# Kernel optimization log

Measured on AMD Instinct MI355X. Metric: run time of the kernel, lower is better.

Reference implementation:

```python
import jax, jax.numpy as jnp
import numpy as np

N, E, G = 20000, 600000, 128
NF, HID, L, H = 16, 128, 4, 4
C = HID // H  # 32 per-head out dim
BN_EPS = 1e-5


def setup_inputs() -> dict:
    key = jax.random.key(0)
    ks = jax.random.split(key, 24)
    inp = {}
    inp['x'] = jax.random.normal(ks[0], (N, NF), dtype=jnp.float32)
    inp['edge_index'] = jax.random.randint(ks[1], (2, E), 0, N, dtype=jnp.int32)
    inp['batch'] = jnp.sort(jax.random.randint(ks[2], (N,), 0, G, dtype=jnp.int32))
    s = 0.05
    inp['emb_w'] = jax.random.normal(ks[3], (NF, HID), dtype=jnp.float32) * s
    inp['emb_b'] = jnp.zeros((HID,), dtype=jnp.float32)
    inp['gat_w'] = jax.random.normal(ks[4], (L, HID, HID), dtype=jnp.float32) * s
    inp['att_src'] = jax.random.normal(ks[5], (L, H, C), dtype=jnp.float32) * s
    inp['att_dst'] = jax.random.normal(ks[6], (L, H, C), dtype=jnp.float32) * s
    inp['gat_b'] = jnp.zeros((L, HID), dtype=jnp.float32)
    inp['bn_gamma'] = jnp.ones((L, HID), dtype=jnp.float32)
    inp['bn_beta'] = jnp.zeros((L, HID), dtype=jnp.float32)
    inp['bn_mean'] = jax.random.normal(ks[7], (L, HID), dtype=jnp.float32) * 0.01
    inp['bn_var'] = jnp.ones((L, HID), dtype=jnp.float32)
    inp['fc1_w'] = jax.random.normal(ks[8], (HID, 64), dtype=jnp.float32) * s
    inp['fc1_b'] = jnp.zeros((64,), dtype=jnp.float32)
    inp['fc2_w'] = jax.random.normal(ks[9], (64, 32), dtype=jnp.float32) * s
    inp['fc2_b'] = jnp.zeros((32,), dtype=jnp.float32)
    inp['bg_w'] = jax.random.normal(ks[10], (32, 1), dtype=jnp.float32) * s
    inp['bg_b'] = jnp.zeros((1,), dtype=jnp.float32)
    return inp


def _gat_layer(x, W, a_src, a_dst, bias, src, dst):
    # PyG GATConv (concat=True, negative_slope=0.2, self-loops already appended)
    h = (x @ W).reshape(N, H, C)                      # [N,H,C]
    s_src = jnp.sum(h * a_src, axis=-1)               # [N,H]
    s_dst = jnp.sum(h * a_dst, axis=-1)               # [N,H]
    e = jax.nn.leaky_relu(s_src[src] + s_dst[dst], 0.2)  # [E+N,H]
    m = jax.ops.segment_max(e, dst, num_segments=N)   # per-dest softmax max
    ex = jnp.exp(e - m[dst])
    denom = jax.ops.segment_sum(ex, dst, num_segments=N)
    alpha = ex / (denom[dst] + 1e-16)                 # [E+N,H]
    msg = h[src] * alpha[:, :, None]                  # [E+N,H,C]
    out = jax.ops.segment_sum(msg, dst, num_segments=N)
    return out.reshape(N, HID) + bias


def reference(x, edge_index, batch, emb_w, emb_b, gat_w, att_src, att_dst, gat_b,
              bn_gamma, bn_beta, bn_mean, bn_var, fc1_w, fc1_b, fc2_w, fc2_b, bg_w, bg_b):
    # add self loops (PyG GATConv default)
    loops = jnp.arange(N, dtype=edge_index.dtype)
    src = jnp.concatenate([edge_index[0], loops])
    dst = jnp.concatenate([edge_index[1], loops])

    h = jax.nn.relu(x @ emb_w + emb_b)
    for l in range(L):
        hn = _gat_layer(h, gat_w[l], att_src[l], att_dst[l], gat_b[l], src, dst)
        hn = (hn - bn_mean[l]) * (bn_gamma[l] / jnp.sqrt(bn_var[l] + BN_EPS)) + bn_beta[l]
        h = h + jax.nn.relu(hn)

    # global mean pool over graphs
    sums = jax.ops.segment_sum(h, batch, num_segments=G)
    cnts = jax.ops.segment_sum(jnp.ones((N,), dtype=h.dtype), batch, num_segments=G)
    g = sums / jnp.maximum(cnts, 1.0)[:, None]        # [G,HID]

    g = jax.nn.relu(g @ fc1_w + fc1_b)
    g = jax.nn.relu(g @ fc2_w + fc2_b)
    out = g @ bg_w + bg_b                              # band_gap head
    return out.squeeze(-1)                             # [G]
```

## Files before the change

### kernel.cpp

```cpp
#include <hip/hip_runtime.h>
#include <math.h>

#define HID 128
#define NF  16
#define NH  4
#define HC  32
#define NLAYERS 4

__global__ void k_count_init(int* __restrict__ counts, int N) {
    int i = blockIdx.x * blockDim.x + threadIdx.x;
    if (i < N) counts[i] = 1;
}

__global__ void k_count_edges(const int* __restrict__ dst, int E, int* __restrict__ counts) {
    int i = blockIdx.x * blockDim.x + threadIdx.x;
    if (i < E) atomicAdd(&counts[dst[i]], 1);
}

__global__ __launch_bounds__(1024) void k_scan(const int* __restrict__ counts,
                                               int* __restrict__ row_ptr, int N) {
    __shared__ int sums[1024];
    const int t = threadIdx.x;
    const int per = (N + 1023) >> 10;
    const int beg = min(t * per, N);
    const int end = min(beg + per, N);
    int s = 0;
    for (int i = beg; i < end; ++i) s += counts[i];
    sums[t] = s;
    __syncthreads();
    for (int off = 1; off < 1024; off <<= 1) {
        int v = (t >= off) ? sums[t - off] : 0;
        __syncthreads();
        sums[t] += v;
        __syncthreads();
    }
    int run = sums[t] - s;
    for (int i = beg; i < end; ++i) { row_ptr[i] = run; run += counts[i]; }
    if (t == 1023) row_ptr[N] = sums[1023];
}

__global__ void k_selfloop(const int* __restrict__ row_ptr, int* __restrict__ col,
                           int* __restrict__ fill, int N) {
    int i = blockIdx.x * blockDim.x + threadIdx.x;
    if (i < N) { col[row_ptr[i]] = i; fill[i] = 1; }
}

__global__ void k_scatter(const int* __restrict__ src, const int* __restrict__ dst, int E,
                          const int* __restrict__ row_ptr, int* __restrict__ fill,
                          int* __restrict__ col) {
    int i = blockIdx.x * blockDim.x + threadIdx.x;
    if (i < E) {
        int d = dst[i];
        int pos = atomicAdd(&fill[d], 1);
        col[row_ptr[d] + pos] = src[i];
    }
}

__global__ void k_bnprep(const float* __restrict__ gat_b, const float* __restrict__ gamma,
                         const float* __restrict__ beta, const float* __restrict__ mean,
                         const float* __restrict__ var,
                         float* __restrict__ scale, float* __restrict__ shift) {
    int i = blockIdx.x * blockDim.x + threadIdx.x;
    if (i < NLAYERS * HID) {
        float sc = gamma[i] / sqrtf(var[i] + 1e-5f);
        scale[i] = sc;
        shift[i] = beta[i] + (gat_b[i] - mean[i]) * sc;
    }
}

__global__ __launch_bounds__(256) void k_embed(const float* __restrict__ x,
                                               const float* __restrict__ w,
                                               const float* __restrict__ b,
                                               float* __restrict__ h, int N) {
    __shared__ float ws_[NF * HID];
    __shared__ float bs[HID];
    const int t = threadIdx.x;
    for (int i = t; i < NF * HID; i += 256) ws_[i] = w[i];
    if (t < HID) bs[t] = b[t];
    __syncthreads();
    const int n = blockIdx.x * 2 + (t >> 7);
    const int j = t & 127;
    if (n >= N) return;
    float a = bs[j];
    const float4* xp = (const float4*)(x + (size_t)n * NF);
#pragma unroll
    for (int q = 0; q < 4; ++q) {
        const float4 xv = xp[q];
        a = fmaf(xv.x, ws_[(q * 4 + 0) * HID + j], a);
        a = fmaf(xv.y, ws_[(q * 4 + 1) * HID + j], a);
        a = fmaf(xv.z, ws_[(q * 4 + 2) * HID + j], a);
        a = fmaf(xv.w, ws_[(q * 4 + 3) * HID + j], a);
    }
    h[(size_t)n * HID + j] = fmaxf(a, 0.f);
}

__global__ __launch_bounds__(256) void k_gemm_attn(
    const float* __restrict__ h, const float* __restrict__ W,
    const float* __restrict__ a_src, const float* __restrict__ a_dst,
    float* __restrict__ hproj, float* __restrict__ ssrc, float* __restrict__ sdst, int N) {
    __shared__ float As[16][34];
    __shared__ float Bs[16][132];
    const int tid = threadIdx.x;
    const int m0 = blockIdx.x * 32;
    const int tx = tid & 15;
    const int ty = tid >> 4;
    float acc[2][8];
#pragma unroll
    for (int i = 0; i < 2; ++i)
#pragma unroll
        for (int j = 0; j < 8; ++j) acc[i][j] = 0.f;

    const int arow = tid >> 3;
    const int ak   = (tid & 7) << 1;
    const int brow = tid >> 4;
    const int bcol = (tid & 15) << 3;
    const int gr = m0 + arow;

    for (int k0 = 0; k0 < HID; k0 += 16) {
        float2 av = make_float2(0.f, 0.f);
        if (gr < N) av = *(const float2*)(h + (size_t)gr * HID + k0 + ak);
        const float4 bv0 = *(const float4*)(W + (k0 + brow) * HID + bcol);
        const float4 bv1 = *(const float4*)(W + (k0 + brow) * HID + bcol + 4);
        __syncthreads();
        As[ak + 0][arow] = av.x;
        As[ak + 1][arow] = av.y;
        *(float4*)&Bs[brow][bcol] = bv0;
        *(float4*)&Bs[brow][bcol + 4] = bv1;
        __syncthreads();
#pragma unroll
        for (int k = 0; k < 16; ++k) {
            const float2 a  = *(const float2*)&As[k][ty << 1];
            const float4 b0 = *(const float4*)&Bs[k][tx << 3];
            const float4 b1 = *(const float4*)&Bs[k][(tx << 3) + 4];
            const float aa[2] = {a.x, a.y};
            const float bb[8] = {b0.x, b0.y, b0.z, b0.w, b1.x, b1.y, b1.z, b1.w};
#pragma unroll
            for (int i = 0; i < 2; ++i)
#pragma unroll
                for (int j = 0; j < 8; ++j) acc[i][j] = fmaf(aa[i], bb[j], acc[i][j]);
        }
    }

    const int head = tx >> 2;
    float asv[8], adv[8];
#pragma unroll
    for (int j = 0; j < 8; ++j) {
        asv[j] = a_src[head * HC + (tx & 3) * 8 + j];
        adv[j] = a_dst[head * HC + (tx & 3) * 8 + j];
    }
#pragma unroll
    for (int i = 0; i < 2; ++i) {
        const int r = m0 + (ty << 1) + i;
        if (r < N) {
            const float4 o0 = make_float4(acc[i][0], acc[i][1], acc[i][2], acc[i][3]);
            const float4 o1 = make_float4(acc[i][4], acc[i][5], acc[i][6], acc[i][7]);
            *(float4*)(hproj + (size_t)r * HID + (tx << 3)) = o0;
            *(float4*)(hproj + (size_t)r * HID + (tx << 3) + 4) = o1;
            float ps = 0.f, pd = 0.f;
#pragma unroll
            for (int j = 0; j < 8; ++j) {
                ps = fmaf(acc[i][j], asv[j], ps);
                pd = fmaf(acc[i][j], adv[j], pd);
            }
            ps += __shfl_xor(ps, 1); ps += __shfl_xor(ps, 2);
            pd += __shfl_xor(pd, 1); pd += __shfl_xor(pd, 2);
            if ((tx & 3) == 0) { ssrc[r * NH + head] = ps; sdst[r * NH + head] = pd; }
        }
    }
}

#define LEAKY(e) ((e) > 0.f ? (e) : 0.2f * (e))
__global__ __launch_bounds__(256) void k_sagg(
    float* __restrict__ h, const float2* __restrict__ hproj2,
    const float4* __restrict__ ssrc4, const float4* __restrict__ sdst4,
    const int* __restrict__ row_ptr, const int* __restrict__ col,
    const float2* __restrict__ scale2, const float2* __restrict__ shift2, int N) {
    __shared__ int   s_col[4][64];
    __shared__ float s_alpha[4][64 * 4];
    const int t = threadIdx.x;
    const int w = t >> 6;
    const int lane = t & 63;
    const int n = blockIdx.x * 4 + w;
    if (n >= N) return;
    const int beg = row_ptr[n], end = row_ptr[n + 1];
    const float4 sd = sdst4[n];

    const int i0 = beg + lane;
    const bool v0 = i0 < end;
    int sn0 = 0;
    float fe0 = -1e30f, fe1 = -1e30f, fe2 = -1e30f, fe3 = -1e30f;
    float M0 = -1e30f, M1 = -1e30f, M2 = -1e30f, M3 = -1e30f;
    if (v0) {
        sn0 = col[i0];
        const float4 ss = ssrc4[sn0];
        fe0 = LEAKY(ss.x + sd.x); fe1 = LEAKY(ss.y + sd.y);
        fe2 = LEAKY(ss.z + sd.z); fe3 = LEAKY(ss.w + sd.w);
        M0 = fe0; M1 = fe1; M2 = fe2; M3 = fe3;
    }
    for (int i = i0 + 64; i < end; i += 64) {
        const float4 ss = ssrc4[col[i]];
        M0 = fmaxf(M0, LEAKY(ss.x + sd.x));
        M1 = fmaxf(M1, LEAKY(ss.y + sd.y));
        M2 = fmaxf(M2, LEAKY(ss.z + sd.z));
        M3 = fmaxf(M3, LEAKY(ss.w + sd.w));
    }
#pragma unroll
    for (int o = 32; o >= 1; o >>= 1) {
        M0 = fmaxf(M0, __shfl_xor(M0, o));
        M1 = fmaxf(M1, __shfl_xor(M1, o));
        M2 = fmaxf(M2, __shfl_xor(M2, o));
        M3 = fmaxf(M3, __shfl_xor(M3, o));
    }
    float S0 = 0.f, S1 = 0.f, S2 = 0.f, S3 = 0.f;
    float t0 = 0.f, t1 = 0.f, t2 = 0.f, t3 = 0.f;
    if (v0) {
        t0 = __expf(fe0 - M0); t1 = __expf(fe1 - M1);
        t2 = __expf(fe2 - M2); t3 = __expf(fe3 - M3);
        S0 = t0; S1 = t1; S2 = t2; S3 = t3;
    }
    for (int i = i0 + 64; i < end; i += 64) {
        const float4 ss = ssrc4[col[i]];
        S0 += __expf(LEAKY(ss.x + sd.x) - M0);
        S1 += __expf(LEAKY(ss.y + sd.y) - M1);
        S2 += __expf(LEAKY(ss.z + sd.z) - M2);
        S3 += __expf(LEAKY(ss.w + sd.w) - M3);
    }
#pragma unroll
    for (int o = 32; o >= 1; o >>= 1) {
        S0 += __shfl_xor(S0, o);
        S1 += __shfl_xor(S1, o);
        S2 += __shfl_xor(S2, o);
        S3 += __shfl_xor(S3, o);
    }
    const float inv0 = 1.f / (S0 + 1e-16f);
    const float inv1 = 1.f / (S1 + 1e-16f);
    const float inv2 = 1.f / (S2 + 1e-16f);
    const float inv3 = 1.f / (S3 + 1e-16f);

    const int hh = lane >> 4;
    float2 acc = make_float2(0.f, 0.f);
    {
        if (v0) {
            s_col[w][lane] = sn0;
            float4 a;
            a.x = t0 * inv0; a.y = t1 * inv1; a.z = t2 * inv2; a.w = t3 * inv3;
            *(float4*)&s_alpha[w][lane << 2] = a;
        }
        asm volatile("s_waitcnt lgkmcnt(0)" ::: "memory");
        const int cnt = min(64, end - beg);
#pragma unroll 4
        for (int j = 0; j < cnt; ++j) {
            const int sn = s_col[w][j];
            const float a = s_alpha[w][(j << 2) | hh];
            const float2 hv = hproj2[sn * 64 + lane];
            acc.x = fmaf(a, hv.x, acc.x);
            acc.y = fmaf(a, hv.y, acc.y);
        }
    }
    for (int c0 = beg + 64; c0 < end; c0 += 64) {
        const int i = c0 + lane;
        if (i < end) {
            const int sn = col[i];
            const float4 ss = ssrc4[sn];
            float4 a;
            a.x = __expf(LEAKY(ss.x + sd.x) - M0) * inv0;
            a.y = __expf(LEAKY(ss.y + sd.y) - M1) * inv1;
            a.z = __expf(LEAKY(ss.z + sd.z) - M2) * inv2;
            a.w = __expf(LEAKY(ss.w + sd.w) - M3) * inv3;
            s_col[w][lane] = sn;
            *(float4*)&s_alpha[w][lane << 2] = a;
        }
        asm volatile("s_waitcnt lgkmcnt(0)" ::: "memory");
        const int cnt = min(64, end - c0);
#pragma unroll 4
        for (int j = 0; j < cnt; ++j) {
            const int sn = s_col[w][j];
            const float a = s_alpha[w][(j << 2) | hh];
            const float2 hv = hproj2[sn * 64 + lane];
            acc.x = fmaf(a, hv.x, acc.x);
            acc.y = fmaf(a, hv.y, acc.y);
        }
    }

    const float2 sc = scale2[lane];
    const float2 sh = shift2[lane];
    float2* hp = (float2*)h + (size_t)n * 64 + lane;
    float2 hv = *hp;
    hv.x += fmaxf(fmaf(acc.x, sc.x, sh.x), 0.f);
    hv.y += fmaxf(fmaf(acc.y, sc.y, sh.y), 0.f);
    *hp = hv;
}

__global__ __launch_bounds__(256) void k_pool(const float4* __restrict__ h4,
                                              const int* __restrict__ batch,
                                              float* __restrict__ gout, int N) {
    __shared__ float4 red[8][32];
    const int g = blockIdx.x;
    const int t = threadIdx.x;
    const int c4 = t & 31, r = t >> 5;
    int lo = 0, hi = N;
    while (lo < hi) { int mid = (lo + hi) >> 1; if (batch[mid] < g) lo = mid + 1; else hi = mid; }
    int lo2 = lo, hi2 = N;
    while (lo2 < hi2) { int mid = (lo2 + hi2) >> 1; if (batch[mid] < g + 1) lo2 = mid + 1; else hi2 = mid; }
    float4 acc = make_float4(0.f, 0.f, 0.f, 0.f);
    for (int i = lo + r; i < lo2; i += 8) {
        const float4 v = h4[(size_t)i * 32 + c4];
        acc.x += v.x; acc.y += v.y; acc.z += v.z; acc.w += v.w;
    }
    red[r][c4] = acc;
    __syncthreads();
    if (r == 0) {
#pragma unroll
        for (int k = 1; k < 8; ++k) {
            const float4 v = red[k][c4];
            acc.x += v.x; acc.y += v.y; acc.z += v.z; acc.w += v.w;
        }
        const float invc = 1.f / fmaxf((float)(lo2 - lo), 1.f);
        float4 o = make_float4(acc.x * invc, acc.y * invc, acc.z * invc, acc.w * invc);
        *((float4*)gout + g * 32 + c4) = o;
    }
}

__global__ void k_head(const float* __restrict__ gin,
                       const float* __restrict__ w1, const float* __restrict__ b1,
                       const float* __restrict__ w2, const float* __restrict__ b2,
                       const float* __restrict__ w3, const float* __restrict__ b3,
                       float* __restrict__ out) {
    __shared__ float l1[64];
    __shared__ float l2[32];
    const int g = blockIdx.x;
    const int t = threadIdx.x;
    const float* gv = gin + g * HID;
    float a = b1[t];
    for (int k = 0; k < HID; ++k) a = fmaf(gv[k], w1[k * 64 + t], a);
    l1[t] = fmaxf(a, 0.f);
    __syncthreads();
    if (t < 32) {
        float a2 = b2[t];
        for (int k = 0; k < 64; ++k) a2 = fmaf(l1[k], w2[k * 32 + t], a2);
        l2[t] = fmaxf(a2, 0.f);
    }
    __syncthreads();
    if (t == 0) {
        float a3 = b3[0];
        for (int k = 0; k < 32; ++k) a3 = fmaf(l2[k], w3[k], a3);
        out[g] = a3;
    }
}

extern "C" void kernel_launch(void* const* d_in, const int* in_sizes, int n_in,
                              void* d_out, int out_size, void* d_ws, size_t ws_size,
                              hipStream_t stream) {
    const float* x        = (const float*)d_in[0];
    const int*   eidx     = (const int*)d_in[1];
    const int*   batch    = (const int*)d_in[2];
    const float* emb_w    = (const float*)d_in[3];
    const float* emb_b    = (const float*)d_in[4];
    const float* gat_w    = (const float*)d_in[5];
    const float* att_src  = (const float*)d_in[6];
    const float* att_dst  = (const float*)d_in[7];
    const float* gat_b    = (const float*)d_in[8];
    const float* bn_gamma = (const float*)d_in[9];
    const float* bn_beta  = (const float*)d_in[10];
    const float* bn_mean  = (const float*)d_in[11];
    const float* bn_var   = (const float*)d_in[12];
    const float* fc1_w    = (const float*)d_in[13];
    const float* fc1_b    = (const float*)d_in[14];
    const float* fc2_w    = (const float*)d_in[15];
    const float* fc2_b    = (const float*)d_in[16];
    const float* bg_w     = (const float*)d_in[17];
    const float* bg_b     = (const float*)d_in[18];
    float* out = (float*)d_out;

    const int N = in_sizes[0] / NF;
    const int E = in_sizes[1] / 2;
    const int G = out_size;

    const int* esrc = eidx;
    const int* edst = eidx + E;

    char* ws = (char*)d_ws;
    size_t off = 0;
    auto alloc = [&](size_t bytes) -> void* {
        void* p = ws + off;
        off += (bytes + 255) & ~(size_t)255;
        return p;
    };
    float*  h       = (float*)alloc((size_t)N * HID * sizeof(float));
    float*  hproj   = (float*)alloc((size_t)N * HID * sizeof(float));
    float*  ssrc    = (float*)alloc((size_t)N * NH * sizeof(float));
    float*  sdst    = (float*)alloc((size_t)N * NH * sizeof(float));
    float*  gpool   = (float*)alloc((size_t)G * HID * sizeof(float));
    float*  bnscale = (float*)alloc((size_t)NLAYERS * HID * sizeof(float));
    float*  bnshift = (float*)alloc((size_t)NLAYERS * HID * sizeof(float));
    int*    row_ptr = (int*)alloc((size_t)(N + 1) * sizeof(int));
    int*    counts  = (int*)alloc((size_t)N * sizeof(int));
    int*    col     = (int*)alloc((size_t)(E + N) * sizeof(int));
    (void)ws_size; (void)n_in;

    const int TB = 256;
    k_count_init<<<(N + TB - 1) / TB, TB, 0, stream>>>(counts, N);
    k_count_edges<<<(E + TB - 1) / TB, TB, 0, stream>>>(edst, E, counts);
    k_scan<<<1, 1024, 0, stream>>>(counts, row_ptr, N);
    k_selfloop<<<(N + TB - 1) / TB, TB, 0, stream>>>(row_ptr, col, counts, N);
    k_scatter<<<(E + TB - 1) / TB, TB, 0, stream>>>(esrc, edst, E, row_ptr, counts, col);

    k_bnprep<<<(NLAYERS * HID + TB - 1) / TB, TB, 0, stream>>>(
        gat_b, bn_gamma, bn_beta, bn_mean, bn_var, bnscale, bnshift);

    k_embed<<<(N + 1) / 2, 256, 0, stream>>>(x, emb_w, emb_b, h, N);

    for (int l = 0; l < NLAYERS; ++l) {
        k_gemm_attn<<<(N + 31) / 32, 256, 0, stream>>>(
            h, gat_w + (size_t)l * HID * HID,
            att_src + (size_t)l * NH * HC, att_dst + (size_t)l * NH * HC,
            hproj, ssrc, sdst, N);
        k_sagg<<<(N + 3) / 4, 256, 0, stream>>>(
            h, (const float2*)hproj, (const float4*)ssrc, (const float4*)sdst,
            row_ptr, col,
            (const float2*)(bnscale + l * HID), (const float2*)(bnshift + l * HID), N);
    }

    k_pool<<<G, 256, 0, stream>>>((const float4*)h, batch, gpool, N);
    k_head<<<G, 64, 0, stream>>>(gpool, fc1_w, fc1_b, fc2_w, fc2_b, bg_w, bg_b, out);
}
```

Baseline: 380.1 us.

## Fuse setup and head kernels, double-buffer GEMM, split edges across half-waves in aggregation

Merges the count-init and BN-prep kernels, folds the self-loop insertion into the scan, and combines pooling with the MLP head, which removes several small launches. The GEMM tile grows to 64 rows with double-buffered shared memory, so each k-step needs one barrier instead of two. The aggregation now has each half-wave gather float4 rows for alternating edges and combines the halves with a cross-lane shuffle. This costs more registers and shared memory in the GEMM, and odd edge counts leave some idle padding lanes in the gather.

```diff
diff --git a/kernel.cpp b/kernel.cpp
--- a/kernel.cpp
+++ b/kernel.cpp
@@ -7,9 +7,18 @@
 #define HC  32
 #define NLAYERS 4
 
-__global__ void k_count_init(int* __restrict__ counts, int N) {
+__global__ void k_init(int* __restrict__ counts, int N,
+                       const float* __restrict__ gat_b, const float* __restrict__ gamma,
+                       const float* __restrict__ beta, const float* __restrict__ mean,
+                       const float* __restrict__ var,
+                       float* __restrict__ scale, float* __restrict__ shift) {
     int i = blockIdx.x * blockDim.x + threadIdx.x;
     if (i < N) counts[i] = 1;
+    if (i < NLAYERS * HID) {
+        float sc = gamma[i] / sqrtf(var[i] + 1e-5f);
+        scale[i] = sc;
+        shift[i] = beta[i] + (gat_b[i] - mean[i]) * sc;
+    }
 }
 
 __global__ void k_count_edges(const int* __restrict__ dst, int E, int* __restrict__ counts) {
@@ -18,7 +27,9 @@
 }
 
 __global__ __launch_bounds__(1024) void k_scan(const int* __restrict__ counts,
-                                               int* __restrict__ row_ptr, int N) {
+                                               int* __restrict__ row_ptr,
+                                               int* __restrict__ col,
+                                               int* __restrict__ fill, int N) {
     __shared__ int sums[1024];
     const int t = threadIdx.x;
     const int per = (N + 1023) >> 10;
@@ -35,14 +46,13 @@
         __syncthreads();
     }
     int run = sums[t] - s;
-    for (int i = beg; i < end; ++i) { row_ptr[i] = run; run += counts[i]; }
+    for (int i = beg; i < end; ++i) {
+        row_ptr[i] = run;
+        col[run] = i;
+        fill[i] = 1;
+        run += counts[i];
+    }
     if (t == 1023) row_ptr[N] = sums[1023];
-}
-
-__global__ void k_selfloop(const int* __restrict__ row_ptr, int* __restrict__ col,
-                           int* __restrict__ fill, int N) {
-    int i = blockIdx.x * blockDim.x + threadIdx.x;
-    if (i < N) { col[row_ptr[i]] = i; fill[i] = 1; }
 }
 
 __global__ void k_scatter(const int* __restrict__ src, const int* __restrict__ dst, int E,
@@ -53,18 +63,6 @@
         int d = dst[i];
         int pos = atomicAdd(&fill[d], 1);
         col[row_ptr[d] + pos] = src[i];
-    }
-}
-
-__global__ void k_bnprep(const float* __restrict__ gat_b, const float* __restrict__ gamma,
-                         const float* __restrict__ beta, const float* __restrict__ mean,
-                         const float* __restrict__ var,
-                         float* __restrict__ scale, float* __restrict__ shift) {
-    int i = blockIdx.x * blockDim.x + threadIdx.x;
-    if (i < NLAYERS * HID) {
-        float sc = gamma[i] / sqrtf(var[i] + 1e-5f);
-        scale[i] = sc;
-        shift[i] = beta[i] + (gat_b[i] - mean[i]) * sc;
     }
 }
 
@@ -98,47 +96,62 @@
     const float* __restrict__ h, const float* __restrict__ W,
     const float* __restrict__ a_src, const float* __restrict__ a_dst,
     float* __restrict__ hproj, float* __restrict__ ssrc, float* __restrict__ sdst, int N) {
-    __shared__ float As[16][34];
-    __shared__ float Bs[16][132];
+    __shared__ float As[2][16][68];
+    __shared__ float Bs[2][16][132];
     const int tid = threadIdx.x;
-    const int m0 = blockIdx.x * 32;
+    const int m0 = blockIdx.x * 64;
     const int tx = tid & 15;
     const int ty = tid >> 4;
-    float acc[2][8];
-#pragma unroll
-    for (int i = 0; i < 2; ++i)
+    float acc[4][8];
+#pragma unroll
+    for (int i = 0; i < 4; ++i)
 #pragma unroll
         for (int j = 0; j < 8; ++j) acc[i][j] = 0.f;
 
-    const int arow = tid >> 3;
-    const int ak   = (tid & 7) << 1;
+    const int arow = tid >> 2;
+    const int ak   = (tid & 3) << 2;
     const int brow = tid >> 4;
     const int bcol = (tid & 15) << 3;
     const int gr = m0 + arow;
-
-    for (int k0 = 0; k0 < HID; k0 += 16) {
-        float2 av = make_float2(0.f, 0.f);
-        if (gr < N) av = *(const float2*)(h + (size_t)gr * HID + k0 + ak);
-        const float4 bv0 = *(const float4*)(W + (k0 + brow) * HID + bcol);
-        const float4 bv1 = *(const float4*)(W + (k0 + brow) * HID + bcol + 4);
+    const float* aptr = h + (size_t)gr * HID + ak;
+    const float* bptr = W + brow * HID + bcol;
+
+    float4 av = (gr < N) ? *(const float4*)aptr : make_float4(0.f, 0.f, 0.f, 0.f);
+    float4 bv0 = *(const float4*)bptr;
+    float4 bv1 = *(const float4*)(bptr + 4);
+    As[0][ak + 0][arow] = av.x; As[0][ak + 1][arow] = av.y;
+    As[0][ak + 2][arow] = av.z; As[0][ak + 3][arow] = av.w;
+    *(float4*)&Bs[0][brow][bcol] = bv0;
+    *(float4*)&Bs[0][brow][bcol + 4] = bv1;
+    __syncthreads();
+
+    for (int k0 = 0; k0 < 8; ++k0) {
+        const int cur = k0 & 1, nxt = cur ^ 1;
+        if (k0 < 7) {
+            av = (gr < N) ? *(const float4*)(aptr + (k0 + 1) * 16)
+                          : make_float4(0.f, 0.f, 0.f, 0.f);
+            bv0 = *(const float4*)(bptr + (size_t)(k0 + 1) * 16 * HID);
+            bv1 = *(const float4*)(bptr + (size_t)(k0 + 1) * 16 * HID + 4);
+        }
+#pragma unroll
+        for (int k = 0; k < 16; ++k) {
+            const float4 a  = *(const float4*)&As[cur][k][ty << 2];
+            const float4 b0 = *(const float4*)&Bs[cur][k][tx << 3];
+            const float4 b1 = *(const float4*)&Bs[cur][k][(tx << 3) + 4];
+            const float aa[4] = {a.x, a.y, a.z, a.w};
+            const float bb[8] = {b0.x, b0.y, b0.z, b0.w, b1.x, b1.y, b1.z, b1.w};
+#pragma unroll
+            for (int i = 0; i < 4; ++i)
+#pragma unroll
+                for (int j = 0; j < 8; ++j) acc[i][j] = fmaf(aa[i], bb[j], acc[i][j]);
+        }
+        if (k0 < 7) {
+            As[nxt][ak + 0][arow] = av.x; As[nxt][ak + 1][arow] = av.y;
+            As[nxt][ak + 2][arow] = av.z; As[nxt][ak + 3][arow] = av.w;
+            *(float4*)&Bs[nxt][brow][bcol] = bv0;
+            *(float4*)&Bs[nxt][brow][bcol + 4] = bv1;
+        }
         __syncthreads();
-        As[ak + 0][arow] = av.x;
-        As[ak + 1][arow] = av.y;
-        *(float4*)&Bs[brow][bcol] = bv0;
-        *(float4*)&Bs[brow][bcol + 4] = bv1;
-        __syncthreads();
-#pragma unroll
-        for (int k = 0; k < 16; ++k) {
-            const float2 a  = *(const float2*)&As[k][ty << 1];
-            const float4 b0 = *(const float4*)&Bs[k][tx << 3];
-            const float4 b1 = *(const float4*)&Bs[k][(tx << 3) + 4];
-            const float aa[2] = {a.x, a.y};
-            const float bb[8] = {b0.x, b0.y, b0.z, b0.w, b1.x, b1.y, b1.z, b1.w};
-#pragma unroll
-            for (int i = 0; i < 2; ++i)
-#pragma unroll
-                for (int j = 0; j < 8; ++j) acc[i][j] = fmaf(aa[i], bb[j], acc[i][j]);
-        }
     }
 
     const int head = tx >> 2;
@@ -149,8 +162,8 @@
         adv[j] = a_dst[head * HC + (tx & 3) * 8 + j];
     }
 #pragma unroll
-    for (int i = 0; i < 2; ++i) {
-        const int r = m0 + (ty << 1) + i;
+    for (int i = 0; i < 4; ++i) {
+        const int r = m0 + (ty << 2) + i;
         if (r < N) {
             const float4 o0 = make_float4(acc[i][0], acc[i][1], acc[i][2], acc[i][3]);
             const float4 o1 = make_float4(acc[i][4], acc[i][5], acc[i][6], acc[i][7]);
@@ -171,12 +184,12 @@
 
 #define LEAKY(e) ((e) > 0.f ? (e) : 0.2f * (e))
 __global__ __launch_bounds__(256) void k_sagg(
-    float* __restrict__ h, const float2* __restrict__ hproj2,
+    float* __restrict__ h, const float4* __restrict__ hproj4,
     const float4* __restrict__ ssrc4, const float4* __restrict__ sdst4,
     const int* __restrict__ row_ptr, const int* __restrict__ col,
-    const float2* __restrict__ scale2, const float2* __restrict__ shift2, int N) {
+    const float4* __restrict__ scale4, const float4* __restrict__ shift4, int N) {
     __shared__ int   s_col[4][64];
-    __shared__ float s_alpha[4][64 * 4];
+    __shared__ float s_alpha[4][256];
     const int t = threadIdx.x;
     const int w = t >> 6;
     const int lane = t & 63;
@@ -237,8 +250,10 @@
     const float inv2 = 1.f / (S2 + 1e-16f);
     const float inv3 = 1.f / (S3 + 1e-16f);
 
-    const int hh = lane >> 4;
-    float2 acc = make_float2(0.f, 0.f);
+    const int c  = lane & 31;
+    const int hh = c >> 3;
+    const int eh = lane >> 5;
+    float4 acc = make_float4(0.f, 0.f, 0.f, 0.f);
     {
         if (v0) {
             s_col[w][lane] = sn0;
@@ -249,12 +264,15 @@
         asm volatile("s_waitcnt lgkmcnt(0)" ::: "memory");
         const int cnt = min(64, end - beg);
 #pragma unroll 4
-        for (int j = 0; j < cnt; ++j) {
-            const int sn = s_col[w][j];
-            const float a = s_alpha[w][(j << 2) | hh];
-            const float2 hv = hproj2[sn * 64 + lane];
+        for (int j2 = 0; j2 < cnt; j2 += 2) {
+            const int j = j2 + eh;
+            float a = 0.f; int sn = s_col[w][0];
+            if (j < cnt) { sn = s_col[w][j]; a = s_alpha[w][(j << 2) | hh]; }
+            const float4 hv = hproj4[(size_t)sn * 32 + c];
             acc.x = fmaf(a, hv.x, acc.x);
             acc.y = fmaf(a, hv.y, acc.y);
+            acc.z = fmaf(a, hv.z, acc.z);
+            acc.w = fmaf(a, hv.w, acc.w);
         }
     }
     for (int c0 = beg + 64; c0 < end; c0 += 64) {
@@ -273,28 +291,45 @@
         asm volatile("s_waitcnt lgkmcnt(0)" ::: "memory");
         const int cnt = min(64, end - c0);
 #pragma unroll 4
-        for (int j = 0; j < cnt; ++j) {
-            const int sn = s_col[w][j];
-            const float a = s_alpha[w][(j << 2) | hh];
-            const float2 hv = hproj2[sn * 64 + lane];
+        for (int j2 = 0; j2 < cnt; j2 += 2) {
+            const int j = j2 + eh;
+            float a = 0.f; int sn = s_col[w][0];
+            if (j < cnt) { sn = s_col[w][j]; a = s_alpha[w][(j << 2) | hh]; }
+            const float4 hv = hproj4[(size_t)sn * 32 + c];
             acc.x = fmaf(a, hv.x, acc.x);
             acc.y = fmaf(a, hv.y, acc.y);
-        }
-    }
-
-    const float2 sc = scale2[lane];
-    const float2 sh = shift2[lane];
-    float2* hp = (float2*)h + (size_t)n * 64 + lane;
-    float2 hv = *hp;
-    hv.x += fmaxf(fmaf(acc.x, sc.x, sh.x), 0.f);
-    hv.y += fmaxf(fmaf(acc.y, sc.y, sh.y), 0.f);
-    *hp = hv;
-}
-
-__global__ __launch_bounds__(256) void k_pool(const float4* __restrict__ h4,
-                                              const int* __restrict__ batch,
-                                              float* __restrict__ gout, int N) {
+            acc.z = fmaf(a, hv.z, acc.z);
+            acc.w = fmaf(a, hv.w, acc.w);
+        }
+    }
+    acc.x += __shfl_xor(acc.x, 32);
+    acc.y += __shfl_xor(acc.y, 32);
+    acc.z += __shfl_xor(acc.z, 32);
+    acc.w += __shfl_xor(acc.w, 32);
+
+    if (lane < 32) {
+        const float4 sc = scale4[c];
+        const float4 sh = shift4[c];
+        float4* hp = (float4*)h + (size_t)n * 32 + c;
+        float4 hv = *hp;
+        hv.x += fmaxf(fmaf(acc.x, sc.x, sh.x), 0.f);
+        hv.y += fmaxf(fmaf(acc.y, sc.y, sh.y), 0.f);
+        hv.z += fmaxf(fmaf(acc.z, sc.z, sh.z), 0.f);
+        hv.w += fmaxf(fmaf(acc.w, sc.w, sh.w), 0.f);
+        *hp = hv;
+    }
+}
+
+__global__ __launch_bounds__(256) void k_poolhead(
+    const float4* __restrict__ h4, const int* __restrict__ batch,
+    const float* __restrict__ w1, const float* __restrict__ b1,
+    const float* __restrict__ w2, const float* __restrict__ b2,
+    const float* __restrict__ w3, const float* __restrict__ b3,
+    float* __restrict__ out, int N) {
     __shared__ float4 red[8][32];
+    __shared__ float gp[HID];
+    __shared__ float l1[64];
+    __shared__ float l2[32];
     const int g = blockIdx.x;
     const int t = threadIdx.x;
     const int c4 = t & 31, r = t >> 5;
@@ -317,23 +352,14 @@
         }
         const float invc = 1.f / fmaxf((float)(lo2 - lo), 1.f);
         float4 o = make_float4(acc.x * invc, acc.y * invc, acc.z * invc, acc.w * invc);
-        *((float4*)gout + g * 32 + c4) = o;
-    }
-}
-
-__global__ void k_head(const float* __restrict__ gin,
-                       const float* __restrict__ w1, const float* __restrict__ b1,
-                       const float* __restrict__ w2, const float* __restrict__ b2,
-                       const float* __restrict__ w3, const float* __restrict__ b3,
-                       float* __restrict__ out) {
-    __shared__ float l1[64];
-    __shared__ float l2[32];
-    const int g = blockIdx.x;
-    const int t = threadIdx.x;
-    const float* gv = gin + g * HID;
-    float a = b1[t];
-    for (int k = 0; k < HID; ++k) a = fmaf(gv[k], w1[k * 64 + t], a);
-    l1[t] = fmaxf(a, 0.f);
+        *(float4*)&gp[c4 << 2] = o;
+    }
+    __syncthreads();
+    if (t < 64) {
+        float a = b1[t];
+        for (int k = 0; k < HID; ++k) a = fmaf(gp[k], w1[k * 64 + t], a);
+        l1[t] = fmaxf(a, 0.f);
+    }
     __syncthreads();
     if (t < 32) {
         float a2 = b2[t];
@@ -390,7 +416,6 @@
     float*  hproj   = (float*)alloc((size_t)N * HID * sizeof(float));
     float*  ssrc    = (float*)alloc((size_t)N * NH * sizeof(float));
     float*  sdst    = (float*)alloc((size_t)N * NH * sizeof(float));
-    float*  gpool   = (float*)alloc((size_t)G * HID * sizeof(float));
     float*  bnscale = (float*)alloc((size_t)NLAYERS * HID * sizeof(float));
     float*  bnshift = (float*)alloc((size_t)NLAYERS * HID * sizeof(float));
     int*    row_ptr = (int*)alloc((size_t)(N + 1) * sizeof(int));
@@ -399,28 +424,25 @@
     (void)ws_size; (void)n_in;
 
     const int TB = 256;
-    k_count_init<<<(N + TB - 1) / TB, TB, 0, stream>>>(counts, N);
+    k_init<<<(N + TB - 1) / TB, TB, 0, stream>>>(counts, N, gat_b, bn_gamma, bn_beta,
+                                                 bn_mean, bn_var, bnscale, bnshift);
     k_count_edges<<<(E + TB - 1) / TB, TB, 0, stream>>>(edst, E, counts);
-    k_scan<<<1, 1024, 0, stream>>>(counts, row_ptr, N);
-    k_selfloop<<<(N + TB - 1) / TB, TB, 0, stream>>>(row_ptr, col, counts, N);
+    k_scan<<<1, 1024, 0, stream>>>(counts, row_ptr, col, counts, N);
     k_scatter<<<(E + TB - 1) / TB, TB, 0, stream>>>(esrc, edst, E, row_ptr, counts, col);
 
-    k_bnprep<<<(NLAYERS * HID + TB - 1) / TB, TB, 0, stream>>>(
-        gat_b, bn_gamma, bn_beta, bn_mean, bn_var, bnscale, bnshift);
-
     k_embed<<<(N + 1) / 2, 256, 0, stream>>>(x, emb_w, emb_b, h, N);
 
     for (int l = 0; l < NLAYERS; ++l) {
-        k_gemm_attn<<<(N + 31) / 32, 256, 0, stream>>>(
+        k_gemm_attn<<<(N + 63) / 64, 256, 0, stream>>>(
             h, gat_w + (size_t)l * HID * HID,
             att_src + (size_t)l * NH * HC, att_dst + (size_t)l * NH * HC,
             hproj, ssrc, sdst, N);
         k_sagg<<<(N + 3) / 4, 256, 0, stream>>>(
-            h, (const float2*)hproj, (const float4*)ssrc, (const float4*)sdst,
+            h, (const float4*)hproj, (const float4*)ssrc, (const float4*)sdst,
             row_ptr, col,
-            (const float2*)(bnscale + l * HID), (const float2*)(bnshift + l * HID), N);
-    }
-
-    k_pool<<<G, 256, 0, stream>>>((const float4*)h, batch, gpool, N);
-    k_head<<<G, 64, 0, stream>>>(gpool, fc1_w, fc1_b, fc2_w, fc2_b, bg_w, bg_b, out);
-}
+            (const float4*)(bnscale + l * HID), (const float4*)(bnshift + l * HID), N);
+    }
+
+    k_poolhead<<<G, 256, 0, stream>>>((const float4*)h, batch,
+                                      fc1_w, fc1_b, fc2_w, fc2_b, bg_w, bg_b, out, N);
+}
```

Result: slower. 390.8 us (+2.8%).
